# Kernel tuning notes

Hardware: AMD Instinct MI355X
Metric: run time of the kernel (lower is better)

Reference implementation:

```python
import jax, jax.numpy as jnp
import numpy as np

B, C, L = 8, 256, 2048
RED = 8
CQK = C // RED  # 32


def setup_inputs() -> dict:
    key = jax.random.key(0)
    ks = jax.random.split(key, 8)
    s = 0.05
    x = jax.random.normal(ks[0], (B, C, L), dtype=jnp.float32)
    Wq = jax.random.normal(ks[1], (CQK, C), dtype=jnp.float32) * s
    bq = jax.random.normal(ks[2], (CQK,), dtype=jnp.float32) * s
    Wk = jax.random.normal(ks[3], (CQK, C), dtype=jnp.float32) * s
    bk = jax.random.normal(ks[4], (CQK,), dtype=jnp.float32) * s
    Wv = jax.random.normal(ks[5], (C, C), dtype=jnp.float32) * s
    bv = jax.random.normal(ks[6], (C,), dtype=jnp.float32) * s
    gamma = jnp.asarray([0.5], dtype=jnp.float32)  # learned scalar (init 0 in torch)
    return {"x": x, "Wq": Wq, "bq": bq, "Wk": Wk, "bk": bk, "Wv": Wv, "bv": bv, "gamma": gamma}


def reference(x, Wq, bq, Wk, bk, Wv, bv, gamma):
    # 1x1 Conv1d == channel-mixing matmul: [O,C] x [B,C,L] -> [B,O,L]
    q = jnp.einsum('oc,bcl->bol', Wq, x) + bq[:, None]   # [B,CQK,L]
    k = jnp.einsum('oc,bcl->bol', Wk, x) + bk[:, None]   # [B,CQK,L]
    v = jnp.einsum('oc,bcl->bol', Wv, x) + bv[:, None]   # [B,C,L]
    # attn[b,i,j] = softmax_j( q(:,i) . k(:,j) )  -- NOTE: no 1/sqrt(d) scaling
    scores = jnp.einsum('bci,bcj->bij', q, k)            # [B,L,L]
    attn = jax.nn.softmax(scores, axis=-1)
    # out[b,c,i] = sum_j v[b,c,j] * attn[b,i,j]
    out = jnp.einsum('bcj,bij->bci', v, attn)            # [B,C,L]
    return gamma[0] * out + x
```

## Files before the change

### kernel.cpp

```cpp
#include <hip/hip_runtime.h>

#define B 8
#define C 256
#define L 2048
#define CQK 32
#define SSEG 4
#define JSEG (L / SSEG)
#define NT (JSEG / 32)
#define SM_SHIFT 20.0f

typedef unsigned short u16;
typedef __attribute__((ext_vector_type(8))) short bf8;
typedef __attribute__((ext_vector_type(4))) float f4;

__device__ __forceinline__ u16 f2bf(float f) {
    union { float f; unsigned u; } v; v.f = f;
    unsigned r = v.u + 0x7FFFu + ((v.u >> 16) & 1u);
    return (u16)(r >> 16);
}
__device__ __forceinline__ float bfl(unsigned u) {
    union { unsigned u; float f; } v; v.u = u << 16; return v.f;
}
__device__ __forceinline__ float bfh(unsigned u) {
    union { unsigned u; float f; } v; v.u = u & 0xFFFF0000u; return v.f;
}

__device__ __forceinline__ void gld16(const u16* gp, u16* lp) {
    auto* g1 = (const __attribute__((address_space(1))) u16*)gp;
    auto* l3 = (__attribute__((address_space(3))) u16*)lp;
    __builtin_amdgcn_global_load_lds(g1, l3, 16, 0, 0);
}
__device__ __forceinline__ void wait_vm0() {
    asm volatile("s_waitcnt vmcnt(0)" ::: "memory");
    __builtin_amdgcn_sched_barrier(0);
}
__device__ __forceinline__ void wait_lgkm0() {
    asm volatile("s_waitcnt lgkmcnt(0)" ::: "memory");
    __builtin_amdgcn_sched_barrier(0);
}
__device__ __forceinline__ void bar() {
    __builtin_amdgcn_sched_barrier(0);
    __builtin_amdgcn_s_barrier();
    __builtin_amdgcn_sched_barrier(0);
}

__global__ __launch_bounds__(256) void wconv(
    const float* __restrict__ Wq, const float* __restrict__ bq,
    const float* __restrict__ Wk, const float* __restrict__ bk,
    const float* __restrict__ Wv, const float* __restrict__ bv,
    u16* __restrict__ Wall, float* __restrict__ ball)
{
    const int idx = (blockIdx.x * 256 + threadIdx.x) * 4;
    const int row = idx >> 8, c = idx & 255;
    const float* s;
    if (row < 32)      s = Wq + row * C + c;
    else if (row < 64) s = Wk + (row - 32) * C + c;
    else               s = Wv + (row - 64) * C + c;
    const float4 v = *(const float4*)s;
    uint2 o;
    o.x = f2bf(v.x) | ((unsigned)f2bf(v.y) << 16);
    o.y = f2bf(v.z) | ((unsigned)f2bf(v.w) << 16);
    *(uint2*)(Wall + idx) = o;
    if (blockIdx.x == 0) {
        for (int i = threadIdx.x; i < 320; i += 256)
            ball[i] = (i < 32) ? bq[i] : (i < 64) ? bk[i - 32] : bv[i - 64];
    }
}

__global__ __launch_bounds__(256) void xconv(const float* __restrict__ x,
                                             u16* __restrict__ xt)
{
    __shared__ float tile[64][65];
    const int b = blockIdx.z, c0 = blockIdx.y * 64, l0 = blockIdx.x * 64;
    const int t = threadIdx.x;
    const int ln = t & 63, w = t >> 6;
#pragma unroll
    for (int i = 0; i < 16; i++) {
        const int c = w * 16 + i;
        tile[c][ln] = x[((size_t)(b * C + c0 + c)) * L + l0 + ln];
    }
    __syncthreads();
    const int lrow = t >> 2, q = t & 3;
    unsigned o[8];
#pragma unroll
    for (int jj = 0; jj < 8; jj++) {
        const float a0 = tile[q * 16 + jj * 2][lrow];
        const float a1 = tile[q * 16 + jj * 2 + 1][lrow];
        o[jj] = f2bf(a0) | ((unsigned)f2bf(a1) << 16);
    }
    u16* dst = xt + ((size_t)(b * L + l0 + lrow)) * 256 + c0 + q * 16;
    *(uint4*)(dst)     = make_uint4(o[0], o[1], o[2], o[3]);
    *(uint4*)(dst + 8) = make_uint4(o[4], o[5], o[6], o[7]);
}

__global__ __launch_bounds__(256) void proj(
    const u16* __restrict__ xt, const u16* __restrict__ Wall,
    const float* __restrict__ ball, u16* __restrict__ qt,
    u16* __restrict__ kt, u16* __restrict__ vv)
{
    __shared__ u16 xlds[64 * 256];
    const int b = blockIdx.y, l0 = blockIdx.x * 64;
    const int t = threadIdx.x, w = t >> 6, ln = t & 63;
    const int lc = ln & 15, g = ln >> 4;

#pragma unroll
    for (int mm = 0; mm < 8; mm++) {
        const int cg = t + mm * 256;
        const int lrow = cg >> 5, phys = cg & 31;
        const int logical = (phys & 24) | ((phys & 7) ^ (lrow & 7));
        gld16(xt + ((size_t)(b * L + l0 + lrow)) * 256 + logical * 8,
              xlds + (size_t)(w * 64 + mm * 256) * 8);
    }
    __syncthreads();

    f4 acc[5][4];
#pragma unroll
    for (int rt = 0; rt < 5; rt++) {
        const int row0 = (w * 5 + rt) * 16 + g * 4;
        const float4 bi = *(const float4*)(ball + row0);
#pragma unroll
        for (int ct = 0; ct < 4; ct++) {
            acc[rt][ct].x = bi.x; acc[rt][ct].y = bi.y;
            acc[rt][ct].z = bi.z; acc[rt][ct].w = bi.w;
        }
    }

#pragma unroll
    for (int k = 0; k < 8; k++) {
        bf8 bfr[4];
#pragma unroll
        for (int ct = 0; ct < 4; ct++) {
            const int lrow = ct * 16 + lc;
            const int lchunk = k * 4 + g;
            const int phys = (lchunk & 24) | ((lchunk & 7) ^ (lrow & 7));
            bfr[ct] = *(const bf8*)(xlds + (size_t)lrow * 256 + phys * 8);
        }
#pragma unroll
        for (int rt = 0; rt < 5; rt++) {
            const bf8 af = *(const bf8*)(Wall +
                (size_t)((w * 5 + rt) * 16 + lc) * 256 + k * 32 + g * 8);
#pragma unroll
            for (int ct = 0; ct < 4; ct++)
                acc[rt][ct] = __builtin_amdgcn_mfma_f32_16x16x32_bf16(
                    af, bfr[ct], acc[rt][ct], 0, 0, 0);
        }
    }

#pragma unroll
    for (int rt = 0; rt < 5; rt++) {
        const int rg = w * 5 + rt;
        const int row0 = rg * 16 + g * 4;
#pragma unroll
        for (int ct = 0; ct < 4; ct++) {
            const int l = l0 + ct * 16 + lc;
            const f4 a = acc[rt][ct];
            if (rg < 2) {
                uint2 o;
                o.x = f2bf(a.x) | ((unsigned)f2bf(a.y) << 16);
                o.y = f2bf(a.z) | ((unsigned)f2bf(a.w) << 16);
                *(uint2*)(qt + ((size_t)(b * L + l)) * 32 + row0) = o;
            } else if (rg < 4) {
                uint2 o;
                o.x = f2bf(a.x) | ((unsigned)f2bf(a.y) << 16);
                o.y = f2bf(a.z) | ((unsigned)f2bf(a.w) << 16);
                *(uint2*)(kt + ((size_t)(b * L + l)) * 32 + (row0 - 32)) = o;
            } else {
                const int c = row0 - 64;
                vv[((size_t)(b * C + c + 0)) * L + l] = f2bf(a.x);
                vv[((size_t)(b * C + c + 1)) * L + l] = f2bf(a.y);
                vv[((size_t)(b * C + c + 2)) * L + l] = f2bf(a.z);
                vv[((size_t)(b * C + c + 3)) * L + l] = f2bf(a.w);
            }
        }
    }
}

__global__ __launch_bounds__(256, 4) void attn(
    const u16* __restrict__ qt, const u16* __restrict__ kt,
    const u16* __restrict__ vv, u16* __restrict__ po,
    float* __restrict__ plsum)
{
    __shared__ u16 vs[2][8192];
    __shared__ u16 ps[64][40];
    __shared__ float fl[64];

    const int b = blockIdx.y, bx = blockIdx.x, sidx = blockIdx.z;
    const int t = threadIdx.x, w = t >> 6, ln = t & 63;
    const int lc = ln & 15, g = ln >> 4;
    const int i0 = bx * 64;
    const int js = sidx * JSEG;
    const int wc0 = w * 64;
    const int tb = (b * 32 + bx) * SSEG + sidx;

    const bf8 qf = *(const bf8*)(qt + ((size_t)(b * L + i0 + w * 16 + lc)) * 32 + g * 8);
    const u16* kbase = kt + ((size_t)b * L) * 32;

    f4 acc[4][4];
    const f4 fz = {0.f, 0.f, 0.f, 0.f};
#pragma unroll
    for (int it = 0; it < 4; it++)
#pragma unroll
        for (int ct = 0; ct < 4; ct++) acc[it][ct] = fz;
    float lsum = 0.f;

    auto stage_v = [&](int buf, int j0) {
#pragma unroll
        for (int mm = 0; mm < 4; mm++) {
            const int cg = t + mm * 256;
            const int c = cg >> 2, ch = cg & 3;
            gld16(vv + ((size_t)(b * C + c)) * L + j0 + ch * 8,
                  vs[buf] + (size_t)(w * 64 + mm * 256) * 8);
        }
    };

    stage_v(0, js);
    bf8 kf0 = *(const bf8*)(kbase + (size_t)(js + lc) * 32 + g * 8);
    bf8 kf1 = *(const bf8*)(kbase + (size_t)(js + 16 + lc) * 32 + g * 8);
    int cur = 0;

#pragma unroll 1
    for (int jt = 0; jt < NT; jt++) {
        wait_vm0();
        bar();
        if (jt + 1 < NT) stage_v(cur ^ 1, js + (jt + 1) * 32);
        bf8 kn0 = kf0, kn1 = kf1;
        if (jt + 1 < NT) {
            const int jn = js + (jt + 1) * 32;
            kn0 = *(const bf8*)(kbase + (size_t)(jn + lc) * 32 + g * 8);
            kn1 = *(const bf8*)(kbase + (size_t)(jn + 16 + lc) * 32 + g * 8);
        }

        const f4 s0 = __builtin_amdgcn_mfma_f32_16x16x32_bf16(kf0, qf, fz, 0, 0, 0);
        const f4 s1 = __builtin_amdgcn_mfma_f32_16x16x32_bf16(kf1, qf, fz, 0, 0, 0);

        const float p0 = __expf(s0.x - SM_SHIFT);
        const float p1 = __expf(s0.y - SM_SHIFT);
        const float p2 = __expf(s0.z - SM_SHIFT);
        const float p3 = __expf(s0.w - SM_SHIFT);
        const float p4 = __expf(s1.x - SM_SHIFT);
        const float p5 = __expf(s1.y - SM_SHIFT);
        const float p6 = __expf(s1.z - SM_SHIFT);
        const float p7 = __expf(s1.w - SM_SHIFT);
        {
            uint2 o;
            o.x = f2bf(p0) | ((unsigned)f2bf(p1) << 16);
            o.y = f2bf(p2) | ((unsigned)f2bf(p3) << 16);
            *(uint2*)(&ps[w * 16 + lc][g * 4]) = o;
            o.x = f2bf(p4) | ((unsigned)f2bf(p5) << 16);
            o.y = f2bf(p6) | ((unsigned)f2bf(p7) << 16);
            *(uint2*)(&ps[w * 16 + lc][16 + g * 4]) = o;
        }
        float psum = ((p0 + p1) + (p2 + p3)) + ((p4 + p5) + (p6 + p7));

        wait_lgkm0();
        bar();

        bf8 vfr[4];
#pragma unroll
        for (int ct = 0; ct < 4; ct++)
            vfr[ct] = *(const bf8*)(vs[cur] + (size_t)(wc0 + ct * 16 + lc) * 32 + g * 8);
        __builtin_amdgcn_s_setprio(1);
#pragma unroll
        for (int it = 0; it < 4; it++) {
            const bf8 paf = *(const bf8*)(&ps[it * 16 + lc][0] + g * 8);
#pragma unroll
            for (int ct = 0; ct < 4; ct++)
                acc[it][ct] = __builtin_amdgcn_mfma_f32_16x16x32_bf16(
                    paf, vfr[ct], acc[it][ct], 0, 0, 0);
        }
        __builtin_amdgcn_s_setprio(0);

        psum += __shfl_xor(psum, 16);
        psum += __shfl_xor(psum, 32);
        lsum += psum;

        kf0 = kn0; kf1 = kn1;
        cur ^= 1;
    }

    fl[w * 16 + lc] = 1.0f / lsum;
    if (g == 0) plsum[(size_t)tb * 64 + w * 16 + lc] = lsum;
    wait_lgkm0();
    bar();
    u16* pob = po + ((size_t)tb * 2048 + t) * 8;
#pragma unroll
    for (int it = 0; it < 4; it++) {
        const float4 iv = *(const float4*)&fl[it * 16 + g * 4];
#pragma unroll
        for (int cp = 0; cp < 2; cp++) {
            const f4 a0 = acc[it][2 * cp];
            const f4 a1 = acc[it][2 * cp + 1];
            uint4 o;
            o.x = f2bf(a0.x * iv.x) | ((unsigned)f2bf(a0.y * iv.y) << 16);
            o.y = f2bf(a0.z * iv.z) | ((unsigned)f2bf(a0.w * iv.w) << 16);
            o.z = f2bf(a1.x * iv.x) | ((unsigned)f2bf(a1.y * iv.y) << 16);
            o.w = f2bf(a1.z * iv.z) | ((unsigned)f2bf(a1.w * iv.w) << 16);
            *(uint4*)(pob + (size_t)(it * 2 + cp) * 2048) = o;
        }
    }
}

__global__ __launch_bounds__(256) void combine(
    const u16* __restrict__ po, const float* __restrict__ plsum,
    const float* __restrict__ x, const float* __restrict__ gamma_p,
    float* __restrict__ out)
{
    __shared__ float raw[4][16];
    __shared__ float wts[4][16];
    const int bx = blockIdx.x, b = blockIdx.y, z = blockIdx.z;
    const int t = threadIdx.x, wq = t >> 6, ln = t & 63;
    const int lc = ln & 15, g = ln >> 4;
    const int tbase = (b * 32 + bx) * SSEG;

    if (t < 64)
        raw[t >> 4][t & 15] = plsum[(size_t)(tbase + (t >> 4)) * 64 + z * 16 + (t & 15)];
    __syncthreads();
    if (t < 16) {
        const float l0 = raw[0][t], l1 = raw[1][t], l2 = raw[2][t], l3 = raw[3][t];
        const float inv = 1.0f / (((l0 + l1) + (l2 + l3)));
        wts[0][t] = l0 * inv; wts[1][t] = l1 * inv;
        wts[2][t] = l2 * inv; wts[3][t] = l3 * inv;
    }
    __syncthreads();

    f4 tot[4];
    const f4 fz = {0.f, 0.f, 0.f, 0.f};
#pragma unroll
    for (int ct = 0; ct < 4; ct++) tot[ct] = fz;

#pragma unroll
    for (int s = 0; s < SSEG; s++) {
        const u16* base = po + ((size_t)(tbase + s) * 2048 + (size_t)z * 2 * 256 + t) * 8;
        const uint4 q0 = *(const uint4*)base;
        const uint4 q1 = *(const uint4*)(base + 2048);
        const float4 wv = *(const float4*)&wts[s][g * 4];
        tot[0].x += wv.x * bfl(q0.x); tot[0].y += wv.y * bfh(q0.x);
        tot[0].z += wv.z * bfl(q0.y); tot[0].w += wv.w * bfh(q0.y);
        tot[1].x += wv.x * bfl(q0.z); tot[1].y += wv.y * bfh(q0.z);
        tot[1].z += wv.z * bfl(q0.w); tot[1].w += wv.w * bfh(q0.w);
        tot[2].x += wv.x * bfl(q1.x); tot[2].y += wv.y * bfh(q1.x);
        tot[2].z += wv.z * bfl(q1.y); tot[2].w += wv.w * bfh(q1.y);
        tot[3].x += wv.x * bfl(q1.z); tot[3].y += wv.y * bfh(q1.z);
        tot[3].z += wv.z * bfl(q1.w); tot[3].w += wv.w * bfh(q1.w);
    }

    const float gmm = gamma_p[0];
#pragma unroll
    for (int ct = 0; ct < 4; ct++) {
        const int c = wq * 64 + ct * 16 + lc;
        const size_t adr = ((size_t)(b * C + c)) * L + bx * 64 + z * 16 + g * 4;
        const float4 xv = *(const float4*)(x + adr);
        float4 o;
        o.x = gmm * tot[ct].x + xv.x;
        o.y = gmm * tot[ct].y + xv.y;
        o.z = gmm * tot[ct].z + xv.z;
        o.w = gmm * tot[ct].w + xv.w;
        *(float4*)(out + adr) = o;
    }
}

extern "C" void kernel_launch(void* const* d_in, const int* in_sizes, int n_in,
                              void* d_out, int out_size, void* d_ws, size_t ws_size,
                              hipStream_t stream) {
    const float* x  = (const float*)d_in[0];
    const float* Wq = (const float*)d_in[1];
    const float* bq = (const float*)d_in[2];
    const float* Wk = (const float*)d_in[3];
    const float* bk = (const float*)d_in[4];
    const float* Wv = (const float*)d_in[5];
    const float* bv = (const float*)d_in[6];
    const float* gm = (const float*)d_in[7];
    float* out = (float*)d_out;

    u16* vvp  = (u16*)d_ws;
    u16* qtp  = vvp + (size_t)B * C * L;
    u16* ktp  = qtp + (size_t)B * L * CQK;
    u16* Wall = ktp + (size_t)B * L * CQK;
    float* ball = (float*)(Wall + 320 * 256);
    u16* xt   = Wall + 320 * 256 + 640;
    u16* po   = xt;
    float* plsum = (float*)(po + (size_t)B * 32 * SSEG * 2048 * 8);

    wconv<<<80, 256, 0, stream>>>(Wq, bq, Wk, bk, Wv, bv, Wall, ball);
    xconv<<<dim3(L / 64, C / 64, B), 256, 0, stream>>>(x, xt);
    proj<<<dim3(L / 64, B), 256, 0, stream>>>(xt, Wall, ball, qtp, ktp, vvp);
    attn<<<dim3(L / 64, B, SSEG), 256, 0, stream>>>(qtp, ktp, vvp, po, plsum);
    combine<<<dim3(L / 64, B, SSEG), 256, 0, stream>>>(po, plsum, x, gm, out);
}
```

Baseline: 72.11 us.

## Use exp2 with prescaled q, swizzle V LDS, remap attn grid, halve proj tile

Several unrelated changes land together. The q projection is prescaled by log2(e) so the softmax can use the raw v_exp_f32 (exp2) instruction instead of __expf. V tiles are staged into LDS with an XOR swizzle to reduce bank conflicts, and the PV loop is reordered so one V fragment is loaded per channel tile. The attention grid is flattened and remapped so blocks sharing the same key/value window run adjacently for better L2 reuse. The proj kernel tile is halved to 32 columns to launch more blocks, at the cost of reloading weights more often.

```diff
diff --git a/kernel.cpp b/kernel.cpp
--- a/kernel.cpp
+++ b/kernel.cpp
@@ -7,7 +7,7 @@
 #define SSEG 4
 #define JSEG (L / SSEG)
 #define NT (JSEG / 32)
-#define SM_SHIFT 20.0f
+#define SM_SHIFT2 28.8539008f
 
 typedef unsigned short u16;
 typedef __attribute__((ext_vector_type(8))) short bf8;
@@ -23,6 +23,11 @@
 }
 __device__ __forceinline__ float bfh(unsigned u) {
     union { unsigned u; float f; } v; v.u = u & 0xFFFF0000u; return v.f;
+}
+__device__ __forceinline__ float ex2(float x) {
+    float r;
+    asm("v_exp_f32 %0, %1" : "=v"(r) : "v"(x));
+    return r;
 }
 
 __device__ __forceinline__ void gld16(const u16* gp, u16* lp) {
@@ -98,13 +103,13 @@
     const float* __restrict__ ball, u16* __restrict__ qt,
     u16* __restrict__ kt, u16* __restrict__ vv)
 {
-    __shared__ u16 xlds[64 * 256];
-    const int b = blockIdx.y, l0 = blockIdx.x * 64;
+    __shared__ u16 xlds[32 * 256];
+    const int b = blockIdx.y, l0 = blockIdx.x * 32;
     const int t = threadIdx.x, w = t >> 6, ln = t & 63;
     const int lc = ln & 15, g = ln >> 4;
 
 #pragma unroll
-    for (int mm = 0; mm < 8; mm++) {
+    for (int mm = 0; mm < 4; mm++) {
         const int cg = t + mm * 256;
         const int lrow = cg >> 5, phys = cg & 31;
         const int logical = (phys & 24) | ((phys & 7) ^ (lrow & 7));
@@ -113,13 +118,13 @@
     }
     __syncthreads();
 
-    f4 acc[5][4];
+    f4 acc[5][2];
 #pragma unroll
     for (int rt = 0; rt < 5; rt++) {
         const int row0 = (w * 5 + rt) * 16 + g * 4;
         const float4 bi = *(const float4*)(ball + row0);
 #pragma unroll
-        for (int ct = 0; ct < 4; ct++) {
+        for (int ct = 0; ct < 2; ct++) {
             acc[rt][ct].x = bi.x; acc[rt][ct].y = bi.y;
             acc[rt][ct].z = bi.z; acc[rt][ct].w = bi.w;
         }
@@ -127,9 +132,9 @@
 
 #pragma unroll
     for (int k = 0; k < 8; k++) {
-        bf8 bfr[4];
-#pragma unroll
-        for (int ct = 0; ct < 4; ct++) {
+        bf8 bfr[2];
+#pragma unroll
+        for (int ct = 0; ct < 2; ct++) {
             const int lrow = ct * 16 + lc;
             const int lchunk = k * 4 + g;
             const int phys = (lchunk & 24) | ((lchunk & 7) ^ (lrow & 7));
@@ -140,24 +145,25 @@
             const bf8 af = *(const bf8*)(Wall +
                 (size_t)((w * 5 + rt) * 16 + lc) * 256 + k * 32 + g * 8);
 #pragma unroll
-            for (int ct = 0; ct < 4; ct++)
+            for (int ct = 0; ct < 2; ct++)
                 acc[rt][ct] = __builtin_amdgcn_mfma_f32_16x16x32_bf16(
                     af, bfr[ct], acc[rt][ct], 0, 0, 0);
         }
     }
 
+    const float Q_SCALE = 1.44269504f;
 #pragma unroll
     for (int rt = 0; rt < 5; rt++) {
         const int rg = w * 5 + rt;
         const int row0 = rg * 16 + g * 4;
 #pragma unroll
-        for (int ct = 0; ct < 4; ct++) {
+        for (int ct = 0; ct < 2; ct++) {
             const int l = l0 + ct * 16 + lc;
             const f4 a = acc[rt][ct];
             if (rg < 2) {
                 uint2 o;
-                o.x = f2bf(a.x) | ((unsigned)f2bf(a.y) << 16);
-                o.y = f2bf(a.z) | ((unsigned)f2bf(a.w) << 16);
+                o.x = f2bf(a.x * Q_SCALE) | ((unsigned)f2bf(a.y * Q_SCALE) << 16);
+                o.y = f2bf(a.z * Q_SCALE) | ((unsigned)f2bf(a.w * Q_SCALE) << 16);
                 *(uint2*)(qt + ((size_t)(b * L + l)) * 32 + row0) = o;
             } else if (rg < 4) {
                 uint2 o;
@@ -184,7 +190,9 @@
     __shared__ u16 ps[64][40];
     __shared__ float fl[64];
 
-    const int b = blockIdx.y, bx = blockIdx.x, sidx = blockIdx.z;
+    const int fid = blockIdx.x;
+    const int win = fid & 31, bx = fid >> 5;
+    const int b = win >> 2, sidx = win & 3;
     const int t = threadIdx.x, w = t >> 6, ln = t & 63;
     const int lc = ln & 15, g = ln >> 4;
     const int i0 = bx * 64;
@@ -193,7 +201,10 @@
     const int tb = (b * 32 + bx) * SSEG + sidx;
 
     const bf8 qf = *(const bf8*)(qt + ((size_t)(b * L + i0 + w * 16 + lc)) * 32 + g * 8);
-    const u16* kbase = kt + ((size_t)b * L) * 32;
+    const u16* kb = kt + ((size_t)(b * L + js + lc)) * 32 + g * 8;
+
+    const int sc = t >> 2, ss = t & 3;
+    const u16* vsrc = vv + ((size_t)(b * C + sc)) * L + js + ((ss ^ (sc & 3)) * 8);
 
     f4 acc[4][4];
     const f4 fz = {0.f, 0.f, 0.f, 0.f};
@@ -203,44 +214,41 @@
         for (int ct = 0; ct < 4; ct++) acc[it][ct] = fz;
     float lsum = 0.f;
 
-    auto stage_v = [&](int buf, int j0) {
-#pragma unroll
-        for (int mm = 0; mm < 4; mm++) {
-            const int cg = t + mm * 256;
-            const int c = cg >> 2, ch = cg & 3;
-            gld16(vv + ((size_t)(b * C + c)) * L + j0 + ch * 8,
-                  vs[buf] + (size_t)(w * 64 + mm * 256) * 8);
-        }
+    auto stage = [&](int buf, int jt) {
+        const u16* s = vsrc + jt * 32;
+        u16* d = &vs[buf][0] + (size_t)(w * 64) * 8;
+#pragma unroll
+        for (int m = 0; m < 4; m++)
+            gld16(s + (size_t)(m * 64) * L, d + (size_t)(m * 256) * 8);
     };
 
-    stage_v(0, js);
-    bf8 kf0 = *(const bf8*)(kbase + (size_t)(js + lc) * 32 + g * 8);
-    bf8 kf1 = *(const bf8*)(kbase + (size_t)(js + 16 + lc) * 32 + g * 8);
+    stage(0, 0);
+    bf8 kf0 = *(const bf8*)(kb);
+    bf8 kf1 = *(const bf8*)(kb + 16 * 32);
     int cur = 0;
 
 #pragma unroll 1
     for (int jt = 0; jt < NT; jt++) {
         wait_vm0();
         bar();
-        if (jt + 1 < NT) stage_v(cur ^ 1, js + (jt + 1) * 32);
+        if (jt + 1 < NT) stage(cur ^ 1, jt + 1);
         bf8 kn0 = kf0, kn1 = kf1;
         if (jt + 1 < NT) {
-            const int jn = js + (jt + 1) * 32;
-            kn0 = *(const bf8*)(kbase + (size_t)(jn + lc) * 32 + g * 8);
-            kn1 = *(const bf8*)(kbase + (size_t)(jn + 16 + lc) * 32 + g * 8);
+            kn0 = *(const bf8*)(kb + (size_t)((jt + 1) * 32) * 32);
+            kn1 = *(const bf8*)(kb + (size_t)((jt + 1) * 32 + 16) * 32);
         }
 
         const f4 s0 = __builtin_amdgcn_mfma_f32_16x16x32_bf16(kf0, qf, fz, 0, 0, 0);
         const f4 s1 = __builtin_amdgcn_mfma_f32_16x16x32_bf16(kf1, qf, fz, 0, 0, 0);
 
-        const float p0 = __expf(s0.x - SM_SHIFT);
-        const float p1 = __expf(s0.y - SM_SHIFT);
-        const float p2 = __expf(s0.z - SM_SHIFT);
-        const float p3 = __expf(s0.w - SM_SHIFT);
-        const float p4 = __expf(s1.x - SM_SHIFT);
-        const float p5 = __expf(s1.y - SM_SHIFT);
-        const float p6 = __expf(s1.z - SM_SHIFT);
-        const float p7 = __expf(s1.w - SM_SHIFT);
+        const float p0 = ex2(s0.x - SM_SHIFT2);
+        const float p1 = ex2(s0.y - SM_SHIFT2);
+        const float p2 = ex2(s0.z - SM_SHIFT2);
+        const float p3 = ex2(s0.w - SM_SHIFT2);
+        const float p4 = ex2(s1.x - SM_SHIFT2);
+        const float p5 = ex2(s1.y - SM_SHIFT2);
+        const float p6 = ex2(s1.z - SM_SHIFT2);
+        const float p7 = ex2(s1.w - SM_SHIFT2);
         {
             uint2 o;
             o.x = f2bf(p0) | ((unsigned)f2bf(p1) << 16);
@@ -251,28 +259,26 @@
             *(uint2*)(&ps[w * 16 + lc][16 + g * 4]) = o;
         }
         float psum = ((p0 + p1) + (p2 + p3)) + ((p4 + p5) + (p6 + p7));
-
-        wait_lgkm0();
-        bar();
-
-        bf8 vfr[4];
-#pragma unroll
-        for (int ct = 0; ct < 4; ct++)
-            vfr[ct] = *(const bf8*)(vs[cur] + (size_t)(wc0 + ct * 16 + lc) * 32 + g * 8);
-        __builtin_amdgcn_s_setprio(1);
-#pragma unroll
-        for (int it = 0; it < 4; it++) {
-            const bf8 paf = *(const bf8*)(&ps[it * 16 + lc][0] + g * 8);
-#pragma unroll
-            for (int ct = 0; ct < 4; ct++)
-                acc[it][ct] = __builtin_amdgcn_mfma_f32_16x16x32_bf16(
-                    paf, vfr[ct], acc[it][ct], 0, 0, 0);
-        }
-        __builtin_amdgcn_s_setprio(0);
-
         psum += __shfl_xor(psum, 16);
         psum += __shfl_xor(psum, 32);
         lsum += psum;
+
+        wait_lgkm0();
+        bar();
+
+        __builtin_amdgcn_s_setprio(1);
+#pragma unroll
+        for (int ct = 0; ct < 4; ct++) {
+            const int c = wc0 + ct * 16 + lc;
+            const bf8 vfr = *(const bf8*)(&vs[cur][0] + (size_t)c * 32 + ((g ^ (c & 3)) * 8));
+#pragma unroll
+            for (int it = 0; it < 4; it++) {
+                const bf8 paf = *(const bf8*)(&ps[it * 16 + lc][0] + g * 8);
+                acc[it][ct] = __builtin_amdgcn_mfma_f32_16x16x32_bf16(
+                    paf, vfr, acc[it][ct], 0, 0, 0);
+            }
+        }
+        __builtin_amdgcn_s_setprio(0);
 
         kf0 = kn0; kf1 = kn1;
         cur ^= 1;
@@ -383,7 +389,7 @@
 
     wconv<<<80, 256, 0, stream>>>(Wq, bq, Wk, bk, Wv, bv, Wall, ball);
     xconv<<<dim3(L / 64, C / 64, B), 256, 0, stream>>>(x, xt);
-    proj<<<dim3(L / 64, B), 256, 0, stream>>>(xt, Wall, ball, qtp, ktp, vvp);
-    attn<<<dim3(L / 64, B, SSEG), 256, 0, stream>>>(qtp, ktp, vvp, po, plsum);
+    proj<<<dim3(L / 32, B), 256, 0, stream>>>(xt, Wall, ball, qtp, ktp, vvp);
+    attn<<<1024, 256, 0, stream>>>(qtp, ktp, vvp, po, plsum);
     combine<<<dim3(L / 64, B, SSEG), 256, 0, stream>>>(po, plsum, x, gm, out);
 }
```

New measurement: 70.67 us. -2.0%, faster.
